# Kernel optimization log

Hardware: AMD Instinct MI355X
Metric: run time of the kernel (lower is better)

Reference implementation:

```python
import jax, jax.numpy as jnp
import numpy as np

B, N, F = 32, 1024, 128
H = 256        # n_hidden and mlp_hidden widths
OUT = 3
BN_EPS = 1e-3  # keras BatchNormalization default epsilon


def setup_inputs() -> dict:
    key = jax.random.key(0)
    ks = jax.random.split(key, 16)
    x = jax.random.normal(ks[0], (B, N, F), dtype=jnp.float32)
    a = (jax.random.uniform(ks[1], (B, N, N)) < 0.02).astype(jnp.float32)
    eps = jnp.zeros((), dtype=jnp.float32)  # trainable GIN epsilon, init 0

    def dense_p(k, fi, fo):
        k1, k2 = jax.random.split(k)
        w = jax.random.normal(k1, (fi, fo), dtype=jnp.float32) * (1.0 / np.sqrt(fi))
        b = jnp.zeros((fo,), dtype=jnp.float32)
        return w, b

    def bn_p(k, f):
        k1, k2 = jax.random.split(k)
        g = 1.0 + 0.1 * jax.random.normal(k1, (f,), dtype=jnp.float32)
        be = 0.1 * jax.random.normal(k2, (f,), dtype=jnp.float32)
        m = 0.1 * jax.random.normal(jax.random.fold_in(k, 7), (f,), dtype=jnp.float32)
        v = jnp.ones((f,), dtype=jnp.float32)
        return g, be, m, v

    w1, b1 = dense_p(ks[2], F, H)
    g1, be1, m1, v1 = bn_p(ks[3], H)
    w2, b2 = dense_p(ks[4], H, H)
    g2, be2, m2, v2 = bn_p(ks[5], H)
    w3, b3 = dense_p(ks[6], H, H)   # final MLP dense -> n_hidden
    g3, be3, m3, v3 = bn_p(ks[7], H)
    wd, bd = dense_p(ks[8], H, OUT)
    return dict(x=x, a=a, eps=eps,
                w1=w1, b1=b1, g1=g1, be1=be1, m1=m1, v1=v1,
                w2=w2, b2=b2, g2=g2, be2=be2, m2=m2, v2=v2,
                w3=w3, b3=b3, g3=g3, be3=be3, m3=m3, v3=v3,
                wd=wd, bd=bd)


def _bn(h, g, be, m, v):
    # inference-mode batchnorm over last (feature) axis
    return (h - m) * (g / jnp.sqrt(v + BN_EPS)) + be


def reference(x, a, eps, w1, b1, g1, be1, m1, v1,
              w2, b2, g2, be2, m2, v2,
              w3, b3, g3, be3, m3, v3, wd, bd):
    # GIN aggregation: (1+eps)*x_i + sum_{j in N(i)} x_j
    agg = jnp.einsum('bij,bjf->bif', a, x)          # [B,N,F]
    h = (1.0 + eps) * x + agg
    # MLP: Dense->BN->relu x2 (mlp_hidden), then Dense(n_hidden)->BN->relu
    h = jax.nn.relu(_bn(h @ w1 + b1, g1, be1, m1, v1))  # [B,N,H]
    h = jax.nn.relu(_bn(h @ w2 + b2, g2, be2, m2, v2))
    h = jax.nn.relu(_bn(h @ w3 + b3, g3, be3, m3, v3))
    # global max pool over nodes, dropout(0) = identity, then head Dense(3)
    pooled = jnp.max(h, axis=1)                      # [B,H]
    return pooled @ wd + bd                          # [B,3]
```

## Files before the change

### kernel.cpp

```cpp
#include <hip/hip_runtime.h>

#define BN_EPS 1e-3f

typedef __attribute__((ext_vector_type(8))) short bf16x8;
typedef __attribute__((ext_vector_type(4))) short short4v;
typedef __attribute__((ext_vector_type(4))) float f32x4;

__device__ __forceinline__ short f2bf(float f) {
    union { float f; unsigned u; } a; a.f = f;
    unsigned r = a.u + 0x7fffu + ((a.u >> 16) & 1u);
    return (short)(r >> 16);
}
__device__ __forceinline__ float bf2f(short s) {
    union { unsigned u; float f; } a;
    a.u = ((unsigned)(unsigned short)s) << 16;
    return a.f;
}

__global__ __launch_bounds__(128) void agg_kernel(
    const float* __restrict__ x, const float* __restrict__ a,
    const float* __restrict__ epsp, float* __restrict__ h0) {
    const int row = blockIdx.x;
    const int b   = row >> 10;
    const int t   = threadIdx.x;

    __shared__ int idx[1024];
    __shared__ int cnt;
    if (t == 0) cnt = 0;
    __syncthreads();

    const float4* arow = reinterpret_cast<const float4*>(a + (size_t)row * 1024);
    float4 v0 = arow[t];
    float4 v1 = arow[t + 128];
    const int j0 = t * 4;
    if (v0.x != 0.f) idx[atomicAdd(&cnt, 1)] = j0 + 0;
    if (v0.y != 0.f) idx[atomicAdd(&cnt, 1)] = j0 + 1;
    if (v0.z != 0.f) idx[atomicAdd(&cnt, 1)] = j0 + 2;
    if (v0.w != 0.f) idx[atomicAdd(&cnt, 1)] = j0 + 3;
    if (v1.x != 0.f) idx[atomicAdd(&cnt, 1)] = 512 + j0 + 0;
    if (v1.y != 0.f) idx[atomicAdd(&cnt, 1)] = 512 + j0 + 1;
    if (v1.z != 0.f) idx[atomicAdd(&cnt, 1)] = 512 + j0 + 2;
    if (v1.w != 0.f) idx[atomicAdd(&cnt, 1)] = 512 + j0 + 3;
    __syncthreads();

    const int n = cnt;
    const float* xb = x + (size_t)b * (1024 * 128);
    float acc = (1.0f + epsp[0]) * xb[(size_t)(row & 1023) * 128 + t];
    for (int q = 0; q < n; ++q) {
        acc += xb[(size_t)idx[q] * 128 + t];
    }
    h0[(size_t)row * 128 + t] = acc;
}

template <int K, bool FUSE_POOL>
__global__ __launch_bounds__(256, 2) void mlp_mfma(
    const float* __restrict__ A, const float* __restrict__ W,
    const float* __restrict__ bias, const float* __restrict__ g,
    const float* __restrict__ be, const float* __restrict__ m,
    const float* __restrict__ v, float* __restrict__ out,
    float* __restrict__ pool) {
    __shared__ __align__(16) short Ah[4][128][8];
    __shared__ __align__(16) short Al[4][128][8];
    __shared__ __align__(16) short Bh[4][128][8];
    __shared__ __align__(16) short Bl[4][128][8];

    const int tid  = threadIdx.x;
    const int lane = tid & 63;
    const int wid  = tid >> 6;
    const int wm = wid >> 1, wn = wid & 1;
    const int row0 = blockIdx.x * 128;
    const int col0 = blockIdx.y * 128;
    const int lr = lane & 15;
    const int kg = lane >> 4;

    const int a_q   = tid & 7;
    const int a_r   = tid >> 3;
    const int a_kg  = a_q >> 1;
    const int a_e0  = (a_q & 1) * 4;
    const int b_c   = tid & 127;
    const int b_kg0 = tid >> 7;

    f32x4 acc[4][4] = {};

    for (int k0 = 0; k0 < K; k0 += 32) {
        f32x4 av[4];
        #pragma unroll
        for (int p = 0; p < 4; ++p)
            av[p] = *reinterpret_cast<const f32x4*>(
                &A[(size_t)(row0 + p * 32 + a_r) * K + k0 + a_q * 4]);
        float wv[2][8];
        #pragma unroll
        for (int q = 0; q < 2; ++q) {
            const int kk = k0 + (b_kg0 + 2 * q) * 8;
            #pragma unroll
            for (int e = 0; e < 8; ++e)
                wv[q][e] = W[(size_t)(kk + e) * 256 + col0 + b_c];
        }
        __syncthreads();
        #pragma unroll
        for (int p = 0; p < 4; ++p) {
            const int rr = p * 32 + a_r;
            float fx[4] = {av[p].x, av[p].y, av[p].z, av[p].w};
            short4v h4, l4;
            #pragma unroll
            for (int e = 0; e < 4; ++e) {
                const short hh = f2bf(fx[e]);
                h4[e] = hh;
                l4[e] = f2bf(fx[e] - bf2f(hh));
            }
            *reinterpret_cast<short4v*>(&Ah[a_kg][rr][a_e0]) = h4;
            *reinterpret_cast<short4v*>(&Al[a_kg][rr][a_e0]) = l4;
        }
        #pragma unroll
        for (int q = 0; q < 2; ++q) {
            bf16x8 h8, l8;
            #pragma unroll
            for (int e = 0; e < 8; ++e) {
                const short hh = f2bf(wv[q][e]);
                h8[e] = hh;
                l8[e] = f2bf(wv[q][e] - bf2f(hh));
            }
            *reinterpret_cast<bf16x8*>(&Bh[b_kg0 + 2 * q][b_c][0]) = h8;
            *reinterpret_cast<bf16x8*>(&Bl[b_kg0 + 2 * q][b_c][0]) = l8;
        }
        __syncthreads();

        bf16x8 ah[4], al[4];
        #pragma unroll
        for (int mi = 0; mi < 4; ++mi) {
            ah[mi] = *reinterpret_cast<const bf16x8*>(&Ah[kg][wm * 64 + mi * 16 + lr][0]);
            al[mi] = *reinterpret_cast<const bf16x8*>(&Al[kg][wm * 64 + mi * 16 + lr][0]);
        }
        #pragma unroll
        for (int ni = 0; ni < 4; ++ni) {
            bf16x8 bh = *reinterpret_cast<const bf16x8*>(&Bh[kg][wn * 64 + ni * 16 + lr][0]);
            bf16x8 bl = *reinterpret_cast<const bf16x8*>(&Bl[kg][wn * 64 + ni * 16 + lr][0]);
            #pragma unroll
            for (int mi = 0; mi < 4; ++mi) {
                acc[mi][ni] = __builtin_amdgcn_mfma_f32_16x16x32_bf16(ah[mi], bh, acc[mi][ni], 0, 0, 0);
                acc[mi][ni] = __builtin_amdgcn_mfma_f32_16x16x32_bf16(ah[mi], bl, acc[mi][ni], 0, 0, 0);
                acc[mi][ni] = __builtin_amdgcn_mfma_f32_16x16x32_bf16(al[mi], bh, acc[mi][ni], 0, 0, 0);
            }
        }
    }

    const int b = row0 >> 10;
    #pragma unroll
    for (int ni = 0; ni < 4; ++ni) {
        const int c = col0 + wn * 64 + ni * 16 + lr;
        const float s  = g[c] * rsqrtf(v[c] + BN_EPS);
        const float tt = be[c] - m[c] * s;
        const float bb = bias[c];
        if (FUSE_POOL) {
            float mx = 0.0f;
            #pragma unroll
            for (int mi = 0; mi < 4; ++mi)
                #pragma unroll
                for (int r = 0; r < 4; ++r)
                    mx = fmaxf(mx, fmaf(acc[mi][ni][r] + bb, s, tt));
            mx = fmaxf(mx, __shfl_xor(mx, 16));
            mx = fmaxf(mx, __shfl_xor(mx, 32));
            if (lane < 16)
                atomicMax((int*)&pool[b * 256 + c], __float_as_int(mx));
        } else {
            #pragma unroll
            for (int mi = 0; mi < 4; ++mi) {
                const int rbase = row0 + wm * 64 + mi * 16 + (lane >> 4) * 4;
                #pragma unroll
                for (int r = 0; r < 4; ++r) {
                    const float val = fmaf(acc[mi][ni][r] + bb, s, tt);
                    out[(size_t)(rbase + r) * 256 + c] = fmaxf(val, 0.f);
                }
            }
        }
    }
}

__global__ __launch_bounds__(256) void pool_init(float* __restrict__ pool) {
    pool[blockIdx.x * 256 + threadIdx.x] = 0.0f;
}

__global__ __launch_bounds__(256) void head_kernel(const float* __restrict__ pool,
                                                   const float* __restrict__ wd,
                                                   const float* __restrict__ bd,
                                                   float* __restrict__ out) {
    const int b = blockIdx.x;
    const int t = threadIdx.x;
    const int w = t >> 6;
    const int lane = t & 63;
    if (w < 3) {
        float s = 0.f;
        #pragma unroll
        for (int k = 0; k < 256; k += 64)
            s += pool[b * 256 + k + lane] * wd[(k + lane) * 3 + w];
        #pragma unroll
        for (int off = 32; off; off >>= 1) s += __shfl_down(s, off);
        if (lane == 0) out[b * 3 + w] = s + bd[w];
    }
}

extern "C" void kernel_launch(void* const* d_in, const int* in_sizes, int n_in,
                              void* d_out, int out_size, void* d_ws, size_t ws_size,
                              hipStream_t stream) {
    const float* x   = (const float*)d_in[0];
    const float* a   = (const float*)d_in[1];
    const float* eps = (const float*)d_in[2];
    const float* w1  = (const float*)d_in[3];
    const float* b1  = (const float*)d_in[4];
    const float* g1  = (const float*)d_in[5];
    const float* be1 = (const float*)d_in[6];
    const float* m1  = (const float*)d_in[7];
    const float* v1  = (const float*)d_in[8];
    const float* w2  = (const float*)d_in[9];
    const float* b2  = (const float*)d_in[10];
    const float* g2  = (const float*)d_in[11];
    const float* be2 = (const float*)d_in[12];
    const float* m2  = (const float*)d_in[13];
    const float* v2  = (const float*)d_in[14];
    const float* w3  = (const float*)d_in[15];
    const float* b3  = (const float*)d_in[16];
    const float* g3  = (const float*)d_in[17];
    const float* be3 = (const float*)d_in[18];
    const float* m3  = (const float*)d_in[19];
    const float* v3  = (const float*)d_in[20];
    const float* wd  = (const float*)d_in[21];
    const float* bd  = (const float*)d_in[22];
    float* out = (float*)d_out;

    char* ws = (char*)d_ws;
    float* h0   = (float*)(ws);
    float* h1   = (float*)(ws + (16u << 20));
    float* h2   = (float*)(ws + (48u << 20));
    float* pool = (float*)(ws + (80u << 20));

    pool_init<<<32, 256, 0, stream>>>(pool);
    agg_kernel<<<32 * 1024, 128, 0, stream>>>(x, a, eps, h0);
    mlp_mfma<128, false><<<dim3(256, 2), 256, 0, stream>>>(h0, w1, b1, g1, be1, m1, v1, h1, nullptr);
    mlp_mfma<256, false><<<dim3(256, 2), 256, 0, stream>>>(h1, w2, b2, g2, be2, m2, v2, h2, nullptr);
    mlp_mfma<256, true ><<<dim3(256, 2), 256, 0, stream>>>(h2, w3, b3, g3, be3, m3, v3, nullptr, pool);
    head_kernel<<<32, 256, 0, stream>>>(pool, wd, bd, out);
}
```

Measured before the change: 320.8 us.

## Fuse three MLP layers into one kernel with pre-split bf16 weights

Replaces the three separate per-layer GEMM kernels with one fused kernel. Each 128-row block keeps its full 256-wide activations in registers and LDS across all three layers, so the h1 and h2 intermediates never round-trip through global memory. A new prep kernel converts the weights once per call into hi/lo bf16 pairs in a packed layout, so the main loop only copies weights into LDS. The cost is higher register pressure from 512-thread blocks holding two 2x8 accumulator sets, fewer blocks (256), and an extra kernel launch.

```diff
diff --git a/kernel.cpp b/kernel.cpp
--- a/kernel.cpp
+++ b/kernel.cpp
@@ -3,7 +3,6 @@
 #define BN_EPS 1e-3f
 
 typedef __attribute__((ext_vector_type(8))) short bf16x8;
-typedef __attribute__((ext_vector_type(4))) short short4v;
 typedef __attribute__((ext_vector_type(4))) float f32x4;
 
 __device__ __forceinline__ short f2bf(float f) {
@@ -52,127 +51,236 @@
     h0[(size_t)row * 128 + t] = acc;
 }
 
-template <int K, bool FUSE_POOL>
-__global__ __launch_bounds__(256, 2) void mlp_mfma(
-    const float* __restrict__ A, const float* __restrict__ W,
-    const float* __restrict__ bias, const float* __restrict__ g,
-    const float* __restrict__ be, const float* __restrict__ m,
-    const float* __restrict__ v, float* __restrict__ out,
+__global__ __launch_bounds__(256) void prep_w(
+    const float* __restrict__ w1, const float* __restrict__ w2,
+    const float* __restrict__ w3, ushort* __restrict__ Wp) {
+    const int k = blockIdx.x;
+    const int c = threadIdx.x;
+    const float* src; int kl, base;
+    if (k < 128)      { src = w1; kl = k;       base = 0; }
+    else if (k < 384) { src = w2; kl = k - 128; base = 65536; }
+    else              { src = w3; kl = k - 384; base = 196608; }
+    const float val = src[(size_t)kl * 256 + c];
+    const short hi = f2bf(val);
+    const short lo = f2bf(val - bf2f(hi));
+    const int off = base + (kl >> 5) * 16384 + ((((kl >> 3) & 3) * 256 + c) * 8) + (kl & 7);
+    Wp[off]        = (ushort)hi;
+    Wp[off + 8192] = (ushort)lo;
+}
+
+__global__ __launch_bounds__(512, 2) void fused_mlp(
+    const float* __restrict__ h0, const ushort* __restrict__ Wp,
+    const float* __restrict__ b1, const float* __restrict__ g1,
+    const float* __restrict__ be1, const float* __restrict__ m1,
+    const float* __restrict__ v1,
+    const float* __restrict__ b2, const float* __restrict__ g2,
+    const float* __restrict__ be2, const float* __restrict__ m2,
+    const float* __restrict__ v2,
+    const float* __restrict__ b3, const float* __restrict__ g3,
+    const float* __restrict__ be3, const float* __restrict__ m3,
+    const float* __restrict__ v3,
     float* __restrict__ pool) {
-    __shared__ __align__(16) short Ah[4][128][8];
-    __shared__ __align__(16) short Al[4][128][8];
-    __shared__ __align__(16) short Bh[4][128][8];
-    __shared__ __align__(16) short Bl[4][128][8];
+    __shared__ __align__(16) ushort Wb[2][4][256][8];
+    __shared__ __align__(16) ushort Ab[2][4][4][32][8];
 
     const int tid  = threadIdx.x;
     const int lane = tid & 63;
     const int wid  = tid >> 6;
-    const int wm = wid >> 1, wn = wid & 1;
+    const int wr   = wid >> 1;
+    const int wn   = wid & 1;
+    const int lr   = lane & 15;
+    const int kg   = lane >> 4;
     const int row0 = blockIdx.x * 128;
-    const int col0 = blockIdx.y * 128;
-    const int lr = lane & 15;
-    const int kg = lane >> 4;
-
-    const int a_q   = tid & 7;
-    const int a_r   = tid >> 3;
-    const int a_kg  = a_q >> 1;
-    const int a_e0  = (a_q & 1) * 4;
-    const int b_c   = tid & 127;
-    const int b_kg0 = tid >> 7;
-
-    f32x4 acc[4][4] = {};
-
-    for (int k0 = 0; k0 < K; k0 += 32) {
-        f32x4 av[4];
-        #pragma unroll
-        for (int p = 0; p < 4; ++p)
-            av[p] = *reinterpret_cast<const f32x4*>(
-                &A[(size_t)(row0 + p * 32 + a_r) * K + k0 + a_q * 4]);
-        float wv[2][8];
-        #pragma unroll
-        for (int q = 0; q < 2; ++q) {
-            const int kk = k0 + (b_kg0 + 2 * q) * 8;
-            #pragma unroll
-            for (int e = 0; e < 8; ++e)
-                wv[q][e] = W[(size_t)(kk + e) * 256 + col0 + b_c];
-        }
-        __syncthreads();
-        #pragma unroll
-        for (int p = 0; p < 4; ++p) {
-            const int rr = p * 32 + a_r;
-            float fx[4] = {av[p].x, av[p].y, av[p].z, av[p].w};
-            short4v h4, l4;
-            #pragma unroll
-            for (int e = 0; e < 4; ++e) {
-                const short hh = f2bf(fx[e]);
-                h4[e] = hh;
-                l4[e] = f2bf(fx[e] - bf2f(hh));
+
+    f32x4 acc1[2][8] = {};
+    f32x4 acc2[2][8] = {};
+
+    const int arow = tid >> 2;
+    const int akq  = tid & 3;
+    const float* aptr = h0 + (size_t)(row0 + arow) * 128 + akq * 8;
+
+    #pragma unroll
+    for (int kc = 0; kc < 4; ++kc) {
+        f32x4 a0 = *reinterpret_cast<const f32x4*>(aptr + kc * 32);
+        f32x4 a1 = *reinterpret_cast<const f32x4*>(aptr + kc * 32 + 4);
+        const f32x4* wsrc = reinterpret_cast<const f32x4*>(Wp + kc * 16384);
+        f32x4 wv0 = wsrc[tid], wv1 = wsrc[512 + tid];
+        f32x4 wv2 = wsrc[1024 + tid], wv3 = wsrc[1536 + tid];
+        __syncthreads();
+        {
+            float av[8] = {a0.x, a0.y, a0.z, a0.w, a1.x, a1.y, a1.z, a1.w};
+            bf16x8 hi, lo;
+            #pragma unroll
+            for (int e = 0; e < 8; ++e) {
+                const short h = f2bf(av[e]);
+                hi[e] = h; lo[e] = f2bf(av[e] - bf2f(h));
             }
-            *reinterpret_cast<short4v*>(&Ah[a_kg][rr][a_e0]) = h4;
-            *reinterpret_cast<short4v*>(&Al[a_kg][rr][a_e0]) = l4;
-        }
-        #pragma unroll
-        for (int q = 0; q < 2; ++q) {
-            bf16x8 h8, l8;
-            #pragma unroll
-            for (int e = 0; e < 8; ++e) {
-                const short hh = f2bf(wv[q][e]);
-                h8[e] = hh;
-                l8[e] = f2bf(wv[q][e] - bf2f(hh));
+            *reinterpret_cast<bf16x8*>(&Ab[0][arow >> 5][akq][arow & 31][0]) = hi;
+            *reinterpret_cast<bf16x8*>(&Ab[1][arow >> 5][akq][arow & 31][0]) = lo;
+        }
+        f32x4* wdst = reinterpret_cast<f32x4*>(Wb);
+        wdst[tid] = wv0; wdst[512 + tid] = wv1;
+        wdst[1024 + tid] = wv2; wdst[1536 + tid] = wv3;
+        __syncthreads();
+
+        bf16x8 ah0 = *reinterpret_cast<bf16x8*>(&Ab[0][wr][kg][lr][0]);
+        bf16x8 al0 = *reinterpret_cast<bf16x8*>(&Ab[1][wr][kg][lr][0]);
+        bf16x8 ah1 = *reinterpret_cast<bf16x8*>(&Ab[0][wr][kg][16 + lr][0]);
+        bf16x8 al1 = *reinterpret_cast<bf16x8*>(&Ab[1][wr][kg][16 + lr][0]);
+        #pragma unroll
+        for (int ni = 0; ni < 8; ++ni) {
+            bf16x8 bh = *reinterpret_cast<bf16x8*>(&Wb[0][kg][wn * 128 + ni * 16 + lr][0]);
+            bf16x8 bl = *reinterpret_cast<bf16x8*>(&Wb[1][kg][wn * 128 + ni * 16 + lr][0]);
+            acc1[0][ni] = __builtin_amdgcn_mfma_f32_16x16x32_bf16(ah0, bh, acc1[0][ni], 0, 0, 0);
+            acc1[0][ni] = __builtin_amdgcn_mfma_f32_16x16x32_bf16(ah0, bl, acc1[0][ni], 0, 0, 0);
+            acc1[0][ni] = __builtin_amdgcn_mfma_f32_16x16x32_bf16(al0, bh, acc1[0][ni], 0, 0, 0);
+            acc1[1][ni] = __builtin_amdgcn_mfma_f32_16x16x32_bf16(ah1, bh, acc1[1][ni], 0, 0, 0);
+            acc1[1][ni] = __builtin_amdgcn_mfma_f32_16x16x32_bf16(ah1, bl, acc1[1][ni], 0, 0, 0);
+            acc1[1][ni] = __builtin_amdgcn_mfma_f32_16x16x32_bf16(al1, bh, acc1[1][ni], 0, 0, 0);
+        }
+    }
+
+    #pragma unroll
+    for (int ni = 0; ni < 8; ++ni) {
+        const int c = wn * 128 + ni * 16 + lr;
+        const float s  = g1[c] * rsqrtf(v1[c] + BN_EPS);
+        const float tt = be1[c] - m1[c] * s;
+        const float bb = b1[c];
+        #pragma unroll
+        for (int mi = 0; mi < 2; ++mi)
+            #pragma unroll
+            for (int r = 0; r < 4; ++r)
+                acc1[mi][ni][r] = fmaxf(fmaf(acc1[mi][ni][r] + bb, s, tt), 0.f);
+    }
+
+    #pragma unroll
+    for (int kc = 0; kc < 8; ++kc) {
+        const f32x4* wsrc = reinterpret_cast<const f32x4*>(Wp + 65536 + kc * 16384);
+        f32x4 wv0 = wsrc[tid], wv1 = wsrc[512 + tid];
+        f32x4 wv2 = wsrc[1024 + tid], wv3 = wsrc[1536 + tid];
+        __syncthreads();
+        if (wn == (kc >> 2)) {
+            #pragma unroll
+            for (int j = 0; j < 2; ++j) {
+                const int ni  = (kc & 3) * 2 + j;
+                const int kgw = j * 2 + (lr >> 3);
+                const int e   = lr & 7;
+                #pragma unroll
+                for (int mi = 0; mi < 2; ++mi)
+                    #pragma unroll
+                    for (int r = 0; r < 4; ++r) {
+                        const float val = acc1[mi][ni][r];
+                        const short h = f2bf(val);
+                        Ab[0][wr][kgw][mi * 16 + kg * 4 + r][e] = (ushort)h;
+                        Ab[1][wr][kgw][mi * 16 + kg * 4 + r][e] = (ushort)f2bf(val - bf2f(h));
+                    }
             }
-            *reinterpret_cast<bf16x8*>(&Bh[b_kg0 + 2 * q][b_c][0]) = h8;
-            *reinterpret_cast<bf16x8*>(&Bl[b_kg0 + 2 * q][b_c][0]) = l8;
-        }
-        __syncthreads();
-
-        bf16x8 ah[4], al[4];
-        #pragma unroll
-        for (int mi = 0; mi < 4; ++mi) {
-            ah[mi] = *reinterpret_cast<const bf16x8*>(&Ah[kg][wm * 64 + mi * 16 + lr][0]);
-            al[mi] = *reinterpret_cast<const bf16x8*>(&Al[kg][wm * 64 + mi * 16 + lr][0]);
-        }
-        #pragma unroll
-        for (int ni = 0; ni < 4; ++ni) {
-            bf16x8 bh = *reinterpret_cast<const bf16x8*>(&Bh[kg][wn * 64 + ni * 16 + lr][0]);
-            bf16x8 bl = *reinterpret_cast<const bf16x8*>(&Bl[kg][wn * 64 + ni * 16 + lr][0]);
-            #pragma unroll
-            for (int mi = 0; mi < 4; ++mi) {
-                acc[mi][ni] = __builtin_amdgcn_mfma_f32_16x16x32_bf16(ah[mi], bh, acc[mi][ni], 0, 0, 0);
-                acc[mi][ni] = __builtin_amdgcn_mfma_f32_16x16x32_bf16(ah[mi], bl, acc[mi][ni], 0, 0, 0);
-                acc[mi][ni] = __builtin_amdgcn_mfma_f32_16x16x32_bf16(al[mi], bh, acc[mi][ni], 0, 0, 0);
+        }
+        f32x4* wdst = reinterpret_cast<f32x4*>(Wb);
+        wdst[tid] = wv0; wdst[512 + tid] = wv1;
+        wdst[1024 + tid] = wv2; wdst[1536 + tid] = wv3;
+        __syncthreads();
+
+        bf16x8 ah0 = *reinterpret_cast<bf16x8*>(&Ab[0][wr][kg][lr][0]);
+        bf16x8 al0 = *reinterpret_cast<bf16x8*>(&Ab[1][wr][kg][lr][0]);
+        bf16x8 ah1 = *reinterpret_cast<bf16x8*>(&Ab[0][wr][kg][16 + lr][0]);
+        bf16x8 al1 = *reinterpret_cast<bf16x8*>(&Ab[1][wr][kg][16 + lr][0]);
+        #pragma unroll
+        for (int ni = 0; ni < 8; ++ni) {
+            bf16x8 bh = *reinterpret_cast<bf16x8*>(&Wb[0][kg][wn * 128 + ni * 16 + lr][0]);
+            bf16x8 bl = *reinterpret_cast<bf16x8*>(&Wb[1][kg][wn * 128 + ni * 16 + lr][0]);
+            acc2[0][ni] = __builtin_amdgcn_mfma_f32_16x16x32_bf16(ah0, bh, acc2[0][ni], 0, 0, 0);
+            acc2[0][ni] = __builtin_amdgcn_mfma_f32_16x16x32_bf16(ah0, bl, acc2[0][ni], 0, 0, 0);
+            acc2[0][ni] = __builtin_amdgcn_mfma_f32_16x16x32_bf16(al0, bh, acc2[0][ni], 0, 0, 0);
+            acc2[1][ni] = __builtin_amdgcn_mfma_f32_16x16x32_bf16(ah1, bh, acc2[1][ni], 0, 0, 0);
+            acc2[1][ni] = __builtin_amdgcn_mfma_f32_16x16x32_bf16(ah1, bl, acc2[1][ni], 0, 0, 0);
+            acc2[1][ni] = __builtin_amdgcn_mfma_f32_16x16x32_bf16(al1, bh, acc2[1][ni], 0, 0, 0);
+        }
+    }
+
+    #pragma unroll
+    for (int ni = 0; ni < 8; ++ni) {
+        const int c = wn * 128 + ni * 16 + lr;
+        const float s  = g2[c] * rsqrtf(v2[c] + BN_EPS);
+        const float tt = be2[c] - m2[c] * s;
+        const float bb = b2[c];
+        #pragma unroll
+        for (int mi = 0; mi < 2; ++mi)
+            #pragma unroll
+            for (int r = 0; r < 4; ++r)
+                acc2[mi][ni][r] = fmaxf(fmaf(acc2[mi][ni][r] + bb, s, tt), 0.f);
+    }
+
+    #pragma unroll
+    for (int mi = 0; mi < 2; ++mi)
+        #pragma unroll
+        for (int ni = 0; ni < 8; ++ni)
+            #pragma unroll
+            for (int r = 0; r < 4; ++r)
+                acc1[mi][ni][r] = 0.f;
+
+    #pragma unroll
+    for (int kc = 0; kc < 8; ++kc) {
+        const f32x4* wsrc = reinterpret_cast<const f32x4*>(Wp + 196608 + kc * 16384);
+        f32x4 wv0 = wsrc[tid], wv1 = wsrc[512 + tid];
+        f32x4 wv2 = wsrc[1024 + tid], wv3 = wsrc[1536 + tid];
+        __syncthreads();
+        if (wn == (kc >> 2)) {
+            #pragma unroll
+            for (int j = 0; j < 2; ++j) {
+                const int ni  = (kc & 3) * 2 + j;
+                const int kgw = j * 2 + (lr >> 3);
+                const int e   = lr & 7;
+                #pragma unroll
+                for (int mi = 0; mi < 2; ++mi)
+                    #pragma unroll
+                    for (int r = 0; r < 4; ++r) {
+                        const float val = acc2[mi][ni][r];
+                        const short h = f2bf(val);
+                        Ab[0][wr][kgw][mi * 16 + kg * 4 + r][e] = (ushort)h;
+                        Ab[1][wr][kgw][mi * 16 + kg * 4 + r][e] = (ushort)f2bf(val - bf2f(h));
+                    }
             }
         }
-    }
-
-    const int b = row0 >> 10;
-    #pragma unroll
-    for (int ni = 0; ni < 4; ++ni) {
-        const int c = col0 + wn * 64 + ni * 16 + lr;
-        const float s  = g[c] * rsqrtf(v[c] + BN_EPS);
-        const float tt = be[c] - m[c] * s;
-        const float bb = bias[c];
-        if (FUSE_POOL) {
-            float mx = 0.0f;
-            #pragma unroll
-            for (int mi = 0; mi < 4; ++mi)
-                #pragma unroll
-                for (int r = 0; r < 4; ++r)
-                    mx = fmaxf(mx, fmaf(acc[mi][ni][r] + bb, s, tt));
-            mx = fmaxf(mx, __shfl_xor(mx, 16));
-            mx = fmaxf(mx, __shfl_xor(mx, 32));
-            if (lane < 16)
-                atomicMax((int*)&pool[b * 256 + c], __float_as_int(mx));
-        } else {
-            #pragma unroll
-            for (int mi = 0; mi < 4; ++mi) {
-                const int rbase = row0 + wm * 64 + mi * 16 + (lane >> 4) * 4;
-                #pragma unroll
-                for (int r = 0; r < 4; ++r) {
-                    const float val = fmaf(acc[mi][ni][r] + bb, s, tt);
-                    out[(size_t)(rbase + r) * 256 + c] = fmaxf(val, 0.f);
-                }
-            }
-        }
+        f32x4* wdst = reinterpret_cast<f32x4*>(Wb);
+        wdst[tid] = wv0; wdst[512 + tid] = wv1;
+        wdst[1024 + tid] = wv2; wdst[1536 + tid] = wv3;
+        __syncthreads();
+
+        bf16x8 ah0 = *reinterpret_cast<bf16x8*>(&Ab[0][wr][kg][lr][0]);
+        bf16x8 al0 = *reinterpret_cast<bf16x8*>(&Ab[1][wr][kg][lr][0]);
+        bf16x8 ah1 = *reinterpret_cast<bf16x8*>(&Ab[0][wr][kg][16 + lr][0]);
+        bf16x8 al1 = *reinterpret_cast<bf16x8*>(&Ab[1][wr][kg][16 + lr][0]);
+        #pragma unroll
+        for (int ni = 0; ni < 8; ++ni) {
+            bf16x8 bh = *reinterpret_cast<bf16x8*>(&Wb[0][kg][wn * 128 + ni * 16 + lr][0]);
+            bf16x8 bl = *reinterpret_cast<bf16x8*>(&Wb[1][kg][wn * 128 + ni * 16 + lr][0]);
+            acc1[0][ni] = __builtin_amdgcn_mfma_f32_16x16x32_bf16(ah0, bh, acc1[0][ni], 0, 0, 0);
+            acc1[0][ni] = __builtin_amdgcn_mfma_f32_16x16x32_bf16(ah0, bl, acc1[0][ni], 0, 0, 0);
+            acc1[0][ni] = __builtin_amdgcn_mfma_f32_16x16x32_bf16(al0, bh, acc1[0][ni], 0, 0, 0);
+            acc1[1][ni] = __builtin_amdgcn_mfma_f32_16x16x32_bf16(ah1, bh, acc1[1][ni], 0, 0, 0);
+            acc1[1][ni] = __builtin_amdgcn_mfma_f32_16x16x32_bf16(ah1, bl, acc1[1][ni], 0, 0, 0);
+            acc1[1][ni] = __builtin_amdgcn_mfma_f32_16x16x32_bf16(al1, bh, acc1[1][ni], 0, 0, 0);
+        }
+    }
+
+    const int b = blockIdx.x >> 3;
+    #pragma unroll
+    for (int ni = 0; ni < 8; ++ni) {
+        const int c = wn * 128 + ni * 16 + lr;
+        const float s  = g3[c] * rsqrtf(v3[c] + BN_EPS);
+        const float tt = be3[c] - m3[c] * s;
+        const float bb = b3[c];
+        float mx = 0.0f;
+        #pragma unroll
+        for (int mi = 0; mi < 2; ++mi)
+            #pragma unroll
+            for (int r = 0; r < 4; ++r)
+                mx = fmaxf(mx, fmaf(acc1[mi][ni][r] + bb, s, tt));
+        mx = fmaxf(mx, __shfl_xor(mx, 16));
+        mx = fmaxf(mx, __shfl_xor(mx, 32));
+        if (lane < 16)
+            atomicMax((int*)&pool[b * 256 + c], __float_as_int(mx));
     }
 }
 
@@ -228,15 +336,16 @@
     float* out = (float*)d_out;
 
     char* ws = (char*)d_ws;
-    float* h0   = (float*)(ws);
-    float* h1   = (float*)(ws + (16u << 20));
-    float* h2   = (float*)(ws + (48u << 20));
-    float* pool = (float*)(ws + (80u << 20));
+    float*  h0   = (float*)(ws);
+    ushort* Wp   = (ushort*)(ws + (16u << 20));
+    float*  pool = (float*)(ws + (17u << 20));
 
     pool_init<<<32, 256, 0, stream>>>(pool);
+    prep_w<<<640, 256, 0, stream>>>(w1, w2, w3, Wp);
     agg_kernel<<<32 * 1024, 128, 0, stream>>>(x, a, eps, h0);
-    mlp_mfma<128, false><<<dim3(256, 2), 256, 0, stream>>>(h0, w1, b1, g1, be1, m1, v1, h1, nullptr);
-    mlp_mfma<256, false><<<dim3(256, 2), 256, 0, stream>>>(h1, w2, b2, g2, be2, m2, v2, h2, nullptr);
-    mlp_mfma<256, true ><<<dim3(256, 2), 256, 0, stream>>>(h2, w3, b3, g3, be3, m3, v3, nullptr, pool);
+    fused_mlp<<<256, 512, 0, stream>>>(h0, Wp,
+        b1, g1, be1, m1, v1,
+        b2, g2, be2, m2, v2,
+        b3, g3, be3, m3, v3, pool);
     head_kernel<<<32, 256, 0, stream>>>(pool, wd, bd, out);
 }
```

Measured after the change: 294.8 us. 8.1% less time.
